# Performance work log

Hardware: AMD Instinct MI355X
Metric: run time of the kernel (lower is better)

The kernel has to match this reference:

```python
import jax, jax.numpy as jnp
import numpy as np

N = 10000       # cells (nodes)
E = 320000      # edges per order (avg degree 32)
H = 256         # args.hidden
HD = 256        # args.h_decoder
K = 10          # args.K propagation hops
ORDER = 2       # args.Order
ALPHA = 0.5
DRNA = 2000
DATAC = 5000


def spmm(row, col, val, x):
    # sparse [N,N] @ dense [N,H] via gather + segment-sum
    return jax.ops.segment_sum(val[:, None] * x[col], row, num_segments=N)


def higcn_prop(h, fw_logits, row, col, val):
    fw = jax.nn.softmax(fw_logits)  # [K+1]
    def step(carry, w):
        xk, acc = carry
        xk = spmm(row, col, val, xk)
        return (xk, acc + w * xk), None
    (_, out), _ = jax.lax.scan(step, (h, fw[0] * h), fw[1:])
    return out


def higcn(x, Wi, bi, fW, Wo, bo, edges):
    # Wi: [ORDER, D, H], bi: [ORDER, H], fW: [ORDER, K+1]
    zs = []
    for i in range(ORDER):
        h = x @ Wi[i] + bi[i]
        row, col, val = edges[i]
        zs.append(higcn_prop(h, fW[i], row, col, val))
    return jnp.concatenate(zs, axis=1) @ Wo + bo


def decoder(z, W1, b1, W2, b2):
    return jax.nn.relu(z @ W1 + b1) @ W2 + b2


def setup_inputs() -> dict:
    key = jax.random.key(0)
    ks = jax.random.split(key, 32)
    f32 = jnp.float32

    def lin(k, fan_in, shape):
        return jax.random.normal(k, shape, dtype=f32) / jnp.sqrt(f32(fan_in))

    fW_init = ALPHA * (1.0 - ALPHA) ** jnp.arange(K + 1, dtype=f32)

    inp = {
        "X_rna": jax.random.normal(ks[0], (N, DRNA), dtype=f32),
        "X_atac": jax.random.normal(ks[1], (N, DATAC), dtype=f32),
        "row1": jax.random.randint(ks[2], (E,), 0, N, dtype=jnp.int32),
        "col1": jax.random.randint(ks[3], (E,), 0, N, dtype=jnp.int32),
        "val1": jax.random.uniform(ks[4], (E,), dtype=f32) / 32.0,
        "row2": jax.random.randint(ks[5], (E,), 0, N, dtype=jnp.int32),
        "col2": jax.random.randint(ks[6], (E,), 0, N, dtype=jnp.int32),
        "val2": jax.random.uniform(ks[7], (E,), dtype=f32) / 32.0,
        # HiGCN rna encoder
        "Wi_rna": lin(ks[8], DRNA, (ORDER, DRNA, H)),
        "bi_rna": jnp.zeros((ORDER, H), f32),
        "fW_rna": jnp.tile(fW_init[None, :], (ORDER, 1)),
        "Wo_rna": lin(ks[9], ORDER * H, (ORDER * H, H)),
        "bo_rna": jnp.zeros((H,), f32),
        # HiGCN atac encoder
        "Wi_atac": lin(ks[10], DATAC, (ORDER, DATAC, H)),
        "bi_atac": jnp.zeros((ORDER, H), f32),
        "fW_atac": jnp.tile(fW_init[None, :], (ORDER, 1)),
        "Wo_atac": lin(ks[11], ORDER * H, (ORDER * H, H)),
        "bo_atac": jnp.zeros((H,), f32),
        # attention fusion
        "Wa": lin(ks[12], 2 * H, (2 * H, 2)),
        "ba": jnp.zeros((2,), f32),
        # decoders
        "Wd1_rna": lin(ks[13], H, (H, HD)),
        "bd1_rna": jnp.zeros((HD,), f32),
        "Wd2_rna": lin(ks[14], HD, (HD, DRNA)),
        "bd2_rna": jnp.zeros((DRNA,), f32),
        "Wd1_atac": lin(ks[15], H, (H, HD)),
        "bd1_atac": jnp.zeros((HD,), f32),
        "Wd2_atac": lin(ks[16], HD, (HD, DATAC)),
        "bd2_atac": jnp.zeros((DATAC,), f32),
    }
    return inp


def reference(X_rna, X_atac, row1, col1, val1, row2, col2, val2,
              Wi_rna, bi_rna, fW_rna, Wo_rna, bo_rna,
              Wi_atac, bi_atac, fW_atac, Wo_atac, bo_atac,
              Wa, ba,
              Wd1_rna, bd1_rna, Wd2_rna, bd2_rna,
              Wd1_atac, bd1_atac, Wd2_atac, bd2_atac):
    edges = [(row1, col1, val1), (row2, col2, val2)]  # HL[1], HL[2]
    z_rna = higcn(X_rna, Wi_rna, bi_rna, fW_rna, Wo_rna, bo_rna, edges)
    z_atac = higcn(X_atac, Wi_atac, bi_atac, fW_atac, Wo_atac, bo_atac, edges)
    attn = jnp.concatenate([z_rna, z_atac], axis=1) @ Wa + ba  # [N,2]
    weight = jax.nn.softmax(attn, axis=1)
    z = weight[:, 0:1] * z_rna + weight[:, 1:2] * z_atac
    rna_rec = decoder(z, Wd1_rna, bd1_rna, Wd2_rna, bd2_rna)
    atac_rec = decoder(z, Wd1_atac, bd1_atac, Wd2_atac, bd2_atac)
    return (z, z_rna, z_atac, weight, rna_rec, atac_rec)
```

## Files before the change

### kernel.cpp

```cpp
#include <hip/hip_runtime.h>
#include <cstdint>
#include <cstddef>

#define NC    10000
#define EE    320000
#define HID   256
#define KHOP  10
#define D_RNA 2000
#define D_ATAC 5000

static inline int cdiv(int a, int b) { return (a + b - 1) / b; }

__global__ void fw_softmax_kernel(const float* __restrict__ fW_rna,
                                  const float* __restrict__ fW_atac,
                                  float* __restrict__ fw_soft) {
    int t = threadIdx.x;
    if (t < 4) {
        const float* src = (t < 2) ? (fW_rna + t * (KHOP + 1))
                                   : (fW_atac + (t - 2) * (KHOP + 1));
        float mx = -1e30f;
        for (int k = 0; k <= KHOP; k++) mx = fmaxf(mx, src[k]);
        float e[KHOP + 1];
        float s = 0.f;
        for (int k = 0; k <= KHOP; k++) { e[k] = expf(src[k] - mx); s += e[k]; }
        float inv = 1.f / s;
        for (int k = 0; k <= KHOP; k++) fw_soft[t * (KHOP + 1) + k] = e[k] * inv;
    }
}

__global__ void hist_kernel(const int* __restrict__ row, int e_count,
                            int* __restrict__ counts) {
    int e = blockIdx.x * blockDim.x + threadIdx.x;
    if (e < e_count) atomicAdd(&counts[row[e]], 1);
}

__global__ __launch_bounds__(1024) void scan_kernel(const int* __restrict__ counts,
                                                    int* __restrict__ row_start,
                                                    int* __restrict__ cursor,
                                                    int n) {
    __shared__ int part[1024];
    int t = threadIdx.x;
    const int PER = (n + 1023) / 1024;
    int base = t * PER;
    int s = 0;
    for (int i = 0; i < PER; i++) {
        int idx = base + i;
        if (idx < n) s += counts[idx];
    }
    part[t] = s;
    __syncthreads();
    for (int off = 1; off < 1024; off <<= 1) {
        int v = (t >= off) ? part[t - off] : 0;
        __syncthreads();
        part[t] += v;
        __syncthreads();
    }
    int run = (t == 0) ? 0 : part[t - 1];
    for (int i = 0; i < PER; i++) {
        int idx = base + i;
        if (idx < n) {
            row_start[idx] = run;
            cursor[idx] = run;
            run += counts[idx];
        }
    }
    if (t == 1023) row_start[n] = part[1023];
}

__global__ void scatter_kernel(const int* __restrict__ row,
                               const int* __restrict__ col,
                               const float* __restrict__ val, int e_count,
                               int* __restrict__ cursor,
                               int2* __restrict__ ev) {
    int e = blockIdx.x * blockDim.x + threadIdx.x;
    if (e < e_count) {
        int p = atomicAdd(&cursor[row[e]], 1);
        ev[p] = make_int2(col[e], __float_as_int(val[e]));
    }
}

__global__ __launch_bounds__(128) void spmm2_kernel(
    const int* __restrict__ rs0, const int* __restrict__ rs1,
    const int2* __restrict__ ev0, const int2* __restrict__ ev1,
    const float4* __restrict__ x0, const float4* __restrict__ x1,
    float4* __restrict__ y0, float4* __restrict__ y1,
    float* __restrict__ zrna, float* __restrict__ zatac,
    const float* __restrict__ fw_soft, int k) {
    int b = blockIdx.x;
    int order = (b >= NC) ? 1 : 0;
    int n = order ? (b - NC) : b;
    const int* rs = order ? rs1 : rs0;
    const int2* ev = order ? ev1 : ev0;
    const float4* x = order ? x1 : x0;
    float4* y = order ? y1 : y0;

    int t = threadIdx.x;
    int s = rs[n];
    int e = rs[n + 1];
    float4 acc = make_float4(0.f, 0.f, 0.f, 0.f);
#pragma unroll 4
    for (int i = s; i < e; i++) {
        int2 cv = ev[i];
        float v = __int_as_float(cv.y);
        float4 xv = x[(size_t)cv.x * 128 + t];
        acc.x += v * xv.x;
        acc.y += v * xv.y;
        acc.z += v * xv.z;
        acc.w += v * xv.w;
    }
    y[(size_t)n * 128 + t] = acc;

    float w;
    float* zp;
    if (t < 64) {
        w = fw_soft[order * (KHOP + 1) + k];
        zp = zrna + (size_t)n * 512 + order * 256 + t * 4;
    } else {
        w = fw_soft[(2 + order) * (KHOP + 1) + k];
        zp = zatac + (size_t)n * 512 + order * 256 + (t - 64) * 4;
    }
    float4 z = *(float4*)zp;
    z.x += w * acc.x;
    z.y += w * acc.y;
    z.z += w * acc.z;
    z.w += w * acc.w;
    *(float4*)zp = z;
}

__global__ __launch_bounds__(256) void attention_kernel(
    const float* __restrict__ z_rna, const float* __restrict__ z_atac,
    const float* __restrict__ Wa, const float* __restrict__ ba,
    float* __restrict__ z, float* __restrict__ weight) {
    int n = blockIdx.x;
    int t = threadIdx.x;
    float zr = z_rna[(size_t)n * 256 + t];
    float za = z_atac[(size_t)n * 256 + t];
    float p0 = zr * Wa[t * 2 + 0] + za * Wa[(256 + t) * 2 + 0];
    float p1 = zr * Wa[t * 2 + 1] + za * Wa[(256 + t) * 2 + 1];
    for (int off = 32; off > 0; off >>= 1) {
        p0 += __shfl_down(p0, off);
        p1 += __shfl_down(p1, off);
    }
    __shared__ float red0[4], red1[4];
    __shared__ float w0s, w1s;
    int wave = t >> 6, lane = t & 63;
    if (lane == 0) { red0[wave] = p0; red1[wave] = p1; }
    __syncthreads();
    if (t == 0) {
        float a0 = red0[0] + red0[1] + red0[2] + red0[3] + ba[0];
        float a1 = red1[0] + red1[1] + red1[2] + red1[3] + ba[1];
        float m = fmaxf(a0, a1);
        float e0 = expf(a0 - m), e1 = expf(a1 - m);
        float inv = 1.f / (e0 + e1);
        w0s = e0 * inv; w1s = e1 * inv;
        weight[(size_t)n * 2 + 0] = w0s;
        weight[(size_t)n * 2 + 1] = w1s;
    }
    __syncthreads();
    z[(size_t)n * 256 + t] = w0s * zr + w1s * za;
}

template <int BM, int BN, int BK, int TM, int TN, bool RELU,
          bool BSPLIT, bool CSPLIT, bool ZINIT>
__global__ __launch_bounds__(256) void gemm_f32(
    const float* __restrict__ A, int lda,
    const float* __restrict__ B0, const float* __restrict__ B1, int ldb,
    const float* __restrict__ bias0, const float* __restrict__ bias1,
    float* __restrict__ C0, float* __restrict__ C1, int ldc,
    float* __restrict__ Z, const float* __restrict__ fwp,
    int M, int N, int K) {
    constexpr int TX = BN / TN;
    constexpr int TY = BM / TM;
    static_assert(TX * TY == 256, "thread tile mismatch");
    constexpr int LDA_S = BM + 4;
    constexpr int LDB_S = BN + 4;
    __shared__ __align__(16) float As[BK * LDA_S];
    __shared__ __align__(16) float Bs[BK * LDB_S];

    const int tid = threadIdx.x;
    int tx, ty;
    if constexpr (TX == 16 && TY == 16) {
        const int wid = tid >> 6, lane = tid & 63;
        tx = (lane & 7) + (wid & 1) * 8;
        ty = (lane >> 3) + ((wid >> 1) & 1) * 8;
    } else {
        tx = tid % TX;
        ty = tid / TX;
    }
    const int m0 = blockIdx.y * BM;
    const int n0 = blockIdx.x * BN;

    constexpr int A_L4 = (BM * BK) / 1024;
    constexpr int B_L4 = (BK * BN) / 1024;
    static_assert(A_L4 >= 1 && B_L4 >= 1, "tile too small for 256 threads");
    constexpr int KV = BK / 4;
    constexpr int NV = BN / 4;

    float acc[TM][TN];
#pragma unroll
    for (int i = 0; i < TM; i++)
#pragma unroll
        for (int j = 0; j < TN; j++) acc[i][j] = 0.f;

    for (int kt = 0; kt < K; kt += BK) {
        float4 a4[A_L4], b4[B_L4];
#pragma unroll
        for (int l = 0; l < A_L4; l++) {
            int idx = tid + l * 256;
            int ar = idx / KV, ak = (idx % KV) * 4;
            int mg = m0 + ar, kg = kt + ak;
            a4[l] = make_float4(0.f, 0.f, 0.f, 0.f);
            if (mg < M && kg < K)
                a4[l] = *(const float4*)(A + (size_t)mg * lda + kg);
        }
#pragma unroll
        for (int l = 0; l < B_L4; l++) {
            int idx = tid + l * 256;
            int br = idx / NV, bc = (idx % NV) * 4;
            int kg = kt + br, ng = n0 + bc;
            b4[l] = make_float4(0.f, 0.f, 0.f, 0.f);
            if (kg < K && ng < N) {
                const float* Bp;
                if constexpr (BSPLIT) {
                    Bp = (ng < 256 ? B0 : B1) + (size_t)kg * ldb + (ng & 255);
                } else {
                    Bp = B0 + (size_t)kg * ldb + ng;
                }
                b4[l] = *(const float4*)Bp;
            }
        }

        __syncthreads();
#pragma unroll
        for (int l = 0; l < A_L4; l++) {
            int idx = tid + l * 256;
            int ar = idx / KV, ak = (idx % KV) * 4;
            As[(ak + 0) * LDA_S + ar] = a4[l].x;
            As[(ak + 1) * LDA_S + ar] = a4[l].y;
            As[(ak + 2) * LDA_S + ar] = a4[l].z;
            As[(ak + 3) * LDA_S + ar] = a4[l].w;
        }
#pragma unroll
        for (int l = 0; l < B_L4; l++) {
            int idx = tid + l * 256;
            int br = idx / NV, bc = (idx % NV) * 4;
            *(float4*)(Bs + br * LDB_S + bc) = b4[l];
        }
        __syncthreads();

#pragma unroll
        for (int kk = 0; kk < BK; kk++) {
            float a[TM], b[TN];
#pragma unroll
            for (int i = 0; i < TM; i += 4)
                *(float4*)&a[i] = *(const float4*)&As[kk * LDA_S + ty * TM + i];
#pragma unroll
            for (int j = 0; j < TN; j += 4)
                *(float4*)&b[j] = *(const float4*)&Bs[kk * LDB_S + tx * TN + j];
#pragma unroll
            for (int i = 0; i < TM; i++)
#pragma unroll
                for (int j = 0; j < TN; j++) acc[i][j] += a[i] * b[j];
        }
    }

    float bb[TN];
#pragma unroll
    for (int j = 0; j < TN; j++) {
        int n = n0 + tx * TN + j;
        if (n < N) {
            if constexpr (BSPLIT)
                bb[j] = (n < 256) ? bias0[n] : bias1[n & 255];
            else
                bb[j] = bias0[n];
        } else
            bb[j] = 0.f;
    }
#pragma unroll
    for (int i = 0; i < TM; i++) {
        int m = m0 + ty * TM + i;
        if (m >= M) continue;
#pragma unroll
        for (int j = 0; j < TN; j += 4) {
            int n = n0 + tx * TN + j;
            if (n >= N) continue;
            float4 v;
            v.x = acc[i][j + 0] + bb[j + 0];
            v.y = acc[i][j + 1] + bb[j + 1];
            v.z = acc[i][j + 2] + bb[j + 2];
            v.w = acc[i][j + 3] + bb[j + 3];
            if (RELU) {
                v.x = fmaxf(v.x, 0.f);
                v.y = fmaxf(v.y, 0.f);
                v.z = fmaxf(v.z, 0.f);
                v.w = fmaxf(v.w, 0.f);
            }
            float* Cp;
            int nc = n;
            if constexpr (CSPLIT) {
                Cp = (n < 256) ? C0 : C1;
                nc = n & 255;
            } else {
                Cp = C0;
            }
            *(float4*)(Cp + (size_t)m * ldc + nc) = v;
            if constexpr (ZINIT) {
                float wz = fwp[(n >> 8) * (KHOP + 1)];
                float4 zv = make_float4(wz * v.x, wz * v.y, wz * v.z, wz * v.w);
                *(float4*)(Z + (size_t)m * 512 + n) = zv;
            }
        }
    }
}

extern "C" void kernel_launch(void* const* d_in, const int* in_sizes, int n_in,
                              void* d_out, int out_size, void* d_ws, size_t ws_size,
                              hipStream_t stream) {
    const float* X_rna   = (const float*)d_in[0];
    const float* X_atac  = (const float*)d_in[1];
    const int*   row_in[2] = {(const int*)d_in[2], (const int*)d_in[5]};
    const int*   col_in[2] = {(const int*)d_in[3], (const int*)d_in[6]};
    const float* val_in[2] = {(const float*)d_in[4], (const float*)d_in[7]};
    const float* Wi_rna  = (const float*)d_in[8];
    const float* bi_rna  = (const float*)d_in[9];
    const float* fW_rna  = (const float*)d_in[10];
    const float* Wo_rna  = (const float*)d_in[11];
    const float* bo_rna  = (const float*)d_in[12];
    const float* Wi_atac = (const float*)d_in[13];
    const float* bi_atac = (const float*)d_in[14];
    const float* fW_atac = (const float*)d_in[15];
    const float* Wo_atac = (const float*)d_in[16];
    const float* bo_atac = (const float*)d_in[17];
    const float* Wa      = (const float*)d_in[18];
    const float* ba      = (const float*)d_in[19];
    const float* Wd1_rna = (const float*)d_in[20];
    const float* bd1_rna = (const float*)d_in[21];
    const float* Wd2_rna = (const float*)d_in[22];
    const float* bd2_rna = (const float*)d_in[23];
    const float* Wd1_atac = (const float*)d_in[24];
    const float* bd1_atac = (const float*)d_in[25];
    const float* Wd2_atac = (const float*)d_in[26];
    const float* bd2_atac = (const float*)d_in[27];

    float* out = (float*)d_out;
    float* o_z        = out;
    float* o_z_rna    = out + 2560000;
    float* o_z_atac   = out + 5120000;
    float* o_weight   = out + 7680000;
    float* o_rna_rec  = out + 7700000;
    float* o_atac_rec = out + 27700000;

    float* xk00  = o_atac_rec;
    float* xk01  = o_atac_rec + 1 * 5120000;
    float* xk10  = o_atac_rec + 2 * 5120000;
    float* xk11  = o_atac_rec + 3 * 5120000;
    float* Zrna  = o_atac_rec + 4 * 5120000;
    float* Zatac = o_atac_rec + 5 * 5120000;

    char* w = (char*)d_ws;
    float* fw_soft = (float*)w;  w += 256;
    float* d1_rna  = (float*)w;  w += (size_t)NC * 256 * 4;
    float* d1_atac = (float*)w;  w += (size_t)NC * 256 * 4;
    int* counts[2]; int* rstart[2]; int* cursor[2]; int2* ev[2];
    for (int o = 0; o < 2; o++) {
        counts[o] = (int*)w;   w += 40960;
        rstart[o] = (int*)w;   w += 40960;
        cursor[o] = (int*)w;   w += 40960;
        ev[o]     = (int2*)w;  w += (size_t)EE * 8;
    }

    fw_softmax_kernel<<<1, 64, 0, stream>>>(fW_rna, fW_atac, fw_soft);

    for (int o = 0; o < 2; o++) {
        hipMemsetAsync(counts[o], 0, NC * sizeof(int), stream);
        hist_kernel<<<cdiv(EE, 256), 256, 0, stream>>>(row_in[o], EE, counts[o]);
        scan_kernel<<<1, 1024, 0, stream>>>(counts[o], rstart[o], cursor[o], NC);
        scatter_kernel<<<cdiv(EE, 256), 256, 0, stream>>>(
            row_in[o], col_in[o], val_in[o], EE, cursor[o], ev[o]);
    }

    {
        dim3 g(4, cdiv(NC, 128));
        gemm_f32<128, 128, 16, 8, 8, false, true, true, true><<<g, 256, 0, stream>>>(
            X_rna, D_RNA, Wi_rna, Wi_rna + (size_t)D_RNA * HID, HID,
            bi_rna, bi_rna + HID,
            xk00, xk10, 512,
            Zrna, fw_soft,
            NC, 512, D_RNA);
        gemm_f32<128, 128, 16, 8, 8, false, true, true, true><<<g, 256, 0, stream>>>(
            X_atac, D_ATAC, Wi_atac, Wi_atac + (size_t)D_ATAC * HID, HID,
            bi_atac, bi_atac + HID,
            xk00 + 256, xk10 + 256, 512,
            Zatac, fw_soft + 2 * (KHOP + 1),
            NC, 512, D_ATAC);
    }

    {
        float* s0 = xk00; float* d0 = xk01;
        float* s1 = xk10; float* d1 = xk11;
        for (int k = 1; k <= KHOP; k++) {
            spmm2_kernel<<<2 * NC, 128, 0, stream>>>(
                rstart[0], rstart[1], ev[0], ev[1],
                (const float4*)s0, (const float4*)s1,
                (float4*)d0, (float4*)d1,
                Zrna, Zatac, fw_soft, k);
            float* t;
            t = s0; s0 = d0; d0 = t;
            t = s1; s1 = d1; d1 = t;
        }
    }

    {
        dim3 g(4, cdiv(NC, 128));
        gemm_f32<128, 64, 16, 8, 4, false, false, false, false><<<g, 256, 0, stream>>>(
            Zrna, 512, Wo_rna, nullptr, HID, bo_rna, nullptr,
            o_z_rna, nullptr, HID, nullptr, nullptr, NC, HID, 512);
        gemm_f32<128, 64, 16, 8, 4, false, false, false, false><<<g, 256, 0, stream>>>(
            Zatac, 512, Wo_atac, nullptr, HID, bo_atac, nullptr,
            o_z_atac, nullptr, HID, nullptr, nullptr, NC, HID, 512);
    }

    attention_kernel<<<NC, 256, 0, stream>>>(o_z_rna, o_z_atac, Wa, ba, o_z, o_weight);

    {
        dim3 g(4, cdiv(NC, 128));
        gemm_f32<128, 128, 16, 8, 8, true, true, true, false><<<g, 256, 0, stream>>>(
            o_z, HID, Wd1_rna, Wd1_atac, HID, bd1_rna, bd1_atac,
            d1_rna, d1_atac, HID, nullptr, nullptr, NC, 512, HID);
    }

    {
        dim3 g1(cdiv(D_RNA, 128), cdiv(NC, 128));
        gemm_f32<128, 128, 16, 8, 8, false, false, false, false><<<g1, 256, 0, stream>>>(
            d1_rna, HID, Wd2_rna, nullptr, D_RNA, bd2_rna, nullptr,
            o_rna_rec, nullptr, D_RNA, nullptr, nullptr, NC, D_RNA, HID);
        dim3 g2(cdiv(D_ATAC, 128), cdiv(NC, 128));
        gemm_f32<128, 128, 16, 8, 8, false, false, false, false><<<g2, 256, 0, stream>>>(
            d1_atac, HID, Wd2_atac, nullptr, D_ATAC, bd2_atac, nullptr,
            o_atac_rec, nullptr, D_ATAC, nullptr, nullptr, NC, D_ATAC, HID);
    }
}
```

Measured before the change: 4.216 ms.

## Split-K the input projection GEMMs and pair the output projection launches

After: 3.730 ms. -11.5%, faster.

```diff
diff --git a/kernel.cpp b/kernel.cpp
--- a/kernel.cpp
+++ b/kernel.cpp
@@ -160,14 +160,37 @@
     z[(size_t)n * 256 + t] = w0s * zr + w1s * za;
 }
 
+__global__ __launch_bounds__(128) void splitk_reduce_kernel(
+    const float4* __restrict__ P,
+    const float* __restrict__ bias0, const float* __restrict__ bias1,
+    float* __restrict__ C0, float* __restrict__ C1,
+    float* __restrict__ Z, const float* __restrict__ fwp, int sk) {
+    int m = blockIdx.x, t = threadIdx.x;
+    size_t idx = (size_t)m * 128 + t;
+    const size_t plane = (size_t)NC * 128;
+    float4 s = P[idx];
+    for (int z = 1; z < sk; z++) {
+        float4 p = P[idx + (size_t)z * plane];
+        s.x += p.x; s.y += p.y; s.z += p.z; s.w += p.w;
+    }
+    int n = t * 4;
+    const float* bp = (t < 64) ? (bias0 + n) : (bias1 + (n - 256));
+    s.x += bp[0]; s.y += bp[1]; s.z += bp[2]; s.w += bp[3];
+    float* Cp = ((t < 64) ? C0 : C1) + (size_t)m * 512 + (n & 255);
+    *(float4*)Cp = s;
+    float wz = fwp[(t >> 6) * (KHOP + 1)];
+    float4 zv = make_float4(wz * s.x, wz * s.y, wz * s.z, wz * s.w);
+    *(float4*)(Z + (size_t)m * 512 + n) = zv;
+}
+
 template <int BM, int BN, int BK, int TM, int TN, bool RELU,
-          bool BSPLIT, bool CSPLIT, bool ZINIT>
+          bool BSPLIT, bool CSPLIT, bool SPLITK, bool PAIR>
 __global__ __launch_bounds__(256) void gemm_f32(
-    const float* __restrict__ A, int lda,
+    const float* __restrict__ A, const float* __restrict__ A1, int lda,
     const float* __restrict__ B0, const float* __restrict__ B1, int ldb,
     const float* __restrict__ bias0, const float* __restrict__ bias1,
     float* __restrict__ C0, float* __restrict__ C1, int ldc,
-    float* __restrict__ Z, const float* __restrict__ fwp,
+    float* __restrict__ P, int Kc,
     int M, int N, int K) {
     constexpr int TX = BN / TN;
     constexpr int TY = BM / TM;
@@ -190,6 +213,19 @@
     const int m0 = blockIdx.y * BM;
     const int n0 = blockIdx.x * BN;
 
+    int kb = 0, ke = K;
+    if constexpr (SPLITK) {
+        kb = blockIdx.z * Kc;
+        ke = min(K, kb + Kc);
+    }
+    const float* Ap = A;
+    const float* Bp0 = B0;
+    const float* biasp = bias0;
+    float* Cp0 = C0;
+    if constexpr (PAIR) {
+        if (blockIdx.z) { Ap = A1; Bp0 = B1; biasp = bias1; Cp0 = C1; }
+    }
+
     constexpr int A_L4 = (BM * BK) / 1024;
     constexpr int B_L4 = (BK * BN) / 1024;
     static_assert(A_L4 >= 1 && B_L4 >= 1, "tile too small for 256 threads");
@@ -202,7 +238,7 @@
 #pragma unroll
         for (int j = 0; j < TN; j++) acc[i][j] = 0.f;
 
-    for (int kt = 0; kt < K; kt += BK) {
+    for (int kt = kb; kt < ke; kt += BK) {
         float4 a4[A_L4], b4[B_L4];
 #pragma unroll
         for (int l = 0; l < A_L4; l++) {
@@ -210,8 +246,8 @@
             int ar = idx / KV, ak = (idx % KV) * 4;
             int mg = m0 + ar, kg = kt + ak;
             a4[l] = make_float4(0.f, 0.f, 0.f, 0.f);
-            if (mg < M && kg < K)
-                a4[l] = *(const float4*)(A + (size_t)mg * lda + kg);
+            if (mg < M && kg < ke)
+                a4[l] = *(const float4*)(Ap + (size_t)mg * lda + kg);
         }
 #pragma unroll
         for (int l = 0; l < B_L4; l++) {
@@ -219,12 +255,12 @@
             int br = idx / NV, bc = (idx % NV) * 4;
             int kg = kt + br, ng = n0 + bc;
             b4[l] = make_float4(0.f, 0.f, 0.f, 0.f);
-            if (kg < K && ng < N) {
+            if (kg < ke && ng < N) {
                 const float* Bp;
                 if constexpr (BSPLIT) {
                     Bp = (ng < 256 ? B0 : B1) + (size_t)kg * ldb + (ng & 255);
                 } else {
-                    Bp = B0 + (size_t)kg * ldb + ng;
+                    Bp = Bp0 + (size_t)kg * ldb + ng;
                 }
                 b4[l] = *(const float4*)Bp;
             }
@@ -264,6 +300,24 @@
         }
     }
 
+    if constexpr (SPLITK) {
+        float* Pp = P + (size_t)blockIdx.z * M * ldc;
+#pragma unroll
+        for (int i = 0; i < TM; i++) {
+            int m = m0 + ty * TM + i;
+            if (m >= M) continue;
+#pragma unroll
+            for (int j = 0; j < TN; j += 4) {
+                int n = n0 + tx * TN + j;
+                if (n >= N) continue;
+                float4 v = make_float4(acc[i][j + 0], acc[i][j + 1],
+                                       acc[i][j + 2], acc[i][j + 3]);
+                *(float4*)(Pp + (size_t)m * ldc + n) = v;
+            }
+        }
+        return;
+    }
+
     float bb[TN];
 #pragma unroll
     for (int j = 0; j < TN; j++) {
@@ -272,7 +326,7 @@
             if constexpr (BSPLIT)
                 bb[j] = (n < 256) ? bias0[n] : bias1[n & 255];
             else
-                bb[j] = bias0[n];
+                bb[j] = biasp[n];
         } else
             bb[j] = 0.f;
     }
@@ -301,14 +355,9 @@
                 Cp = (n < 256) ? C0 : C1;
                 nc = n & 255;
             } else {
-                Cp = C0;
+                Cp = Cp0;
             }
             *(float4*)(Cp + (size_t)m * ldc + nc) = v;
-            if constexpr (ZINIT) {
-                float wz = fwp[(n >> 8) * (KHOP + 1)];
-                float4 zv = make_float4(wz * v.x, wz * v.y, wz * v.z, wz * v.w);
-                *(float4*)(Z + (size_t)m * 512 + n) = zv;
-            }
         }
     }
 }
@@ -356,6 +405,7 @@
     float* xk11  = o_atac_rec + 3 * 5120000;
     float* Zrna  = o_atac_rec + 4 * 5120000;
     float* Zatac = o_atac_rec + 5 * 5120000;
+    float* Pk    = o_rna_rec;
 
     char* w = (char*)d_ws;
     float* fw_soft = (float*)w;  w += 256;
@@ -380,19 +430,25 @@
     }
 
     {
-        dim3 g(4, cdiv(NC, 128));
-        gemm_f32<128, 128, 16, 8, 8, false, true, true, true><<<g, 256, 0, stream>>>(
-            X_rna, D_RNA, Wi_rna, Wi_rna + (size_t)D_RNA * HID, HID,
-            bi_rna, bi_rna + HID,
-            xk00, xk10, 512,
-            Zrna, fw_soft,
-            NC, 512, D_RNA);
-        gemm_f32<128, 128, 16, 8, 8, false, true, true, true><<<g, 256, 0, stream>>>(
-            X_atac, D_ATAC, Wi_atac, Wi_atac + (size_t)D_ATAC * HID, HID,
-            bi_atac, bi_atac + HID,
-            xk00 + 256, xk10 + 256, 512,
-            Zatac, fw_soft + 2 * (KHOP + 1),
-            NC, 512, D_ATAC);
+        dim3 g(4, cdiv(NC, 128), 3);
+        gemm_f32<128, 128, 16, 8, 8, false, true, false, true, false>
+            <<<g, 256, 0, stream>>>(
+                X_rna, nullptr, D_RNA,
+                Wi_rna, Wi_rna + (size_t)D_RNA * HID, HID,
+                nullptr, nullptr, nullptr, nullptr, 512,
+                Pk, 672, NC, 512, D_RNA);
+        splitk_reduce_kernel<<<NC, 128, 0, stream>>>(
+            (const float4*)Pk, bi_rna, bi_rna + HID,
+            xk00, xk10, Zrna, fw_soft, 3);
+        gemm_f32<128, 128, 16, 8, 8, false, true, false, true, false>
+            <<<g, 256, 0, stream>>>(
+                X_atac, nullptr, D_ATAC,
+                Wi_atac, Wi_atac + (size_t)D_ATAC * HID, HID,
+                nullptr, nullptr, nullptr, nullptr, 512,
+                Pk, 1680, NC, 512, D_ATAC);
+        splitk_reduce_kernel<<<NC, 128, 0, stream>>>(
+            (const float4*)Pk, bi_atac, bi_atac + HID,
+            xk00 + 256, xk10 + 256, Zatac, fw_soft + 2 * (KHOP + 1), 3);
     }
 
     {
@@ -411,32 +467,45 @@
     }
 
     {
-        dim3 g(4, cdiv(NC, 128));
-        gemm_f32<128, 64, 16, 8, 4, false, false, false, false><<<g, 256, 0, stream>>>(
-            Zrna, 512, Wo_rna, nullptr, HID, bo_rna, nullptr,
-            o_z_rna, nullptr, HID, nullptr, nullptr, NC, HID, 512);
-        gemm_f32<128, 64, 16, 8, 4, false, false, false, false><<<g, 256, 0, stream>>>(
-            Zatac, 512, Wo_atac, nullptr, HID, bo_atac, nullptr,
-            o_z_atac, nullptr, HID, nullptr, nullptr, NC, HID, 512);
+        dim3 g(4, cdiv(NC, 128), 2);
+        gemm_f32<128, 64, 16, 8, 4, false, false, false, false, true>
+            <<<g, 256, 0, stream>>>(
+                Zrna, Zatac, 512,
+                Wo_rna, Wo_atac, HID,
+                bo_rna, bo_atac,
+                o_z_rna, o_z_atac, HID,
+                nullptr, 0, NC, HID, 512);
     }
 
     attention_kernel<<<NC, 256, 0, stream>>>(o_z_rna, o_z_atac, Wa, ba, o_z, o_weight);
 
     {
-        dim3 g(4, cdiv(NC, 128));
-        gemm_f32<128, 128, 16, 8, 8, true, true, true, false><<<g, 256, 0, stream>>>(
-            o_z, HID, Wd1_rna, Wd1_atac, HID, bd1_rna, bd1_atac,
-            d1_rna, d1_atac, HID, nullptr, nullptr, NC, 512, HID);
+        dim3 g(8, cdiv(NC, 128));
+        gemm_f32<128, 64, 16, 8, 4, true, true, true, false, false>
+            <<<g, 256, 0, stream>>>(
+                o_z, nullptr, HID,
+                Wd1_rna, Wd1_atac, HID,
+                bd1_rna, bd1_atac,
+                d1_rna, d1_atac, HID,
+                nullptr, 0, NC, 512, HID);
     }
 
     {
         dim3 g1(cdiv(D_RNA, 128), cdiv(NC, 128));
-        gemm_f32<128, 128, 16, 8, 8, false, false, false, false><<<g1, 256, 0, stream>>>(
-            d1_rna, HID, Wd2_rna, nullptr, D_RNA, bd2_rna, nullptr,
-            o_rna_rec, nullptr, D_RNA, nullptr, nullptr, NC, D_RNA, HID);
+        gemm_f32<128, 128, 16, 8, 8, false, false, false, false, false>
+            <<<g1, 256, 0, stream>>>(
+                d1_rna, nullptr, HID,
+                Wd2_rna, nullptr, D_RNA,
+                bd2_rna, nullptr,
+                o_rna_rec, nullptr, D_RNA,
+                nullptr, 0, NC, D_RNA, HID);
         dim3 g2(cdiv(D_ATAC, 128), cdiv(NC, 128));
-        gemm_f32<128, 128, 16, 8, 8, false, false, false, false><<<g2, 256, 0, stream>>>(
-            d1_atac, HID, Wd2_atac, nullptr, D_ATAC, bd2_atac, nullptr,
-            o_atac_rec, nullptr, D_ATAC, nullptr, nullptr, NC, D_ATAC, HID);
-    }
-}
+        gemm_f32<128, 128, 16, 8, 8, false, false, false, false, false>
+            <<<g2, 256, 0, stream>>>(
+                d1_atac, nullptr, HID,
+                Wd2_atac, nullptr, D_ATAC,
+                bd2_atac, nullptr,
+                o_atac_rec, nullptr, D_ATAC,
+                nullptr, 0, NC, D_ATAC, HID);
+    }
+}
```
